# Optimization experiments

Measured on AMD Instinct MI355X. Metric: run time of the kernel, lower is better.

The kernel has to match this reference:

```python
import jax, jax.numpy as jnp
import numpy as np

FACTOR = 5  # sampling factor c

def setup_inputs() -> dict:
    key = jax.random.key(0)
    k1, k2, k3, k4 = jax.random.split(key, 4)
    B, H, L, D = 4, 8, 2048, 64
    u = min(max(1, FACTOR * int(np.ceil(np.log(L)))), L)  # sample_k = 40
    return {
        "queries": jax.random.normal(k1, (B, H, L, D), jnp.float32),
        "keys": jax.random.normal(k2, (B, H, L, D), jnp.float32),
        "values": jax.random.normal(k3, (B, H, L, D), jnp.float32),
        "index_sample": jax.random.randint(k4, (L, u), 0, L, jnp.int32),
    }

def reference(queries, keys, values, index_sample):
    B, H, L_Q, D = queries.shape
    L_K = keys.shape[2]
    scale = 1.0 / np.sqrt(D)
    U_part = min(max(1, FACTOR * int(np.ceil(np.log(L_K)))), L_Q)  # n_top queries

    # --- _prob_QK: sampled scores + sparsity measure ---
    # K_sample[b,h,q,s,:] = keys[b,h,index_sample[q,s],:]  -> (B,H,L_Q,u,D)
    K_sample = keys[:, :, index_sample, :]
    QK_sample = jnp.einsum('bhqd,bhqsd->bhqs', queries, K_sample)  # (B,H,L_Q,u)
    M = QK_sample.max(-1) - QK_sample.sum(-1) / L_K                # (B,H,L_Q)
    _, index = jax.lax.top_k(M, U_part)                            # (B,H,U)

    # --- initial context: mean of V for non-selected queries ---
    context = jnp.broadcast_to(values.mean(-2, keepdims=True), (B, H, L_Q, D))

    # --- full attention for the top-U queries only ---
    Q_reduce = jnp.take_along_axis(queries, index[..., None], axis=2)   # (B,H,U,D)
    scores = jnp.einsum('bhud,bhkd->bhuk', Q_reduce, keys) * scale      # (B,H,U,L_K)
    attn = jax.nn.softmax(scores, axis=-1)
    out = jnp.einsum('bhuk,bhkd->bhud', attn, values)                   # (B,H,U,D)

    # --- scatter selected outputs back into the mean context ---
    bi = jnp.arange(B)[:, None, None]
    hi = jnp.arange(H)[None, :, None]
    context = context.at[bi, hi, index].set(out)
    return context
```

## Files before the change

### kernel.cpp

```cpp
#include <hip/hip_runtime.h>
#include <math.h>

#define Bq 4
#define Hh 8
#define Lh 2048
#define Dh 64
#define BH (Bq*Hh)

__global__ __launch_bounds__(256) void kA_M(const float* __restrict__ Q,
                                            const float* __restrict__ K,
                                            const int* __restrict__ idxs,
                                            float* __restrict__ M, int u) {
    int bi = blockIdx.x;
    int xcd = bi & 7, slot = bi >> 3;
    int bh  = xcd * 4 + (slot >> 5);
    int qt  = slot & 31;
    int tid = threadIdx.x;
    int wave = tid >> 6, lane = tid & 63;
    int g = lane >> 2, c = lane & 3;
    int q = qt * 64 + wave * 16 + g;
    long gq = (long)bh * Lh + q;

    const float* qrow = Q + gq * Dh;
    float4 qf[4];
#pragma unroll
    for (int jj = 0; jj < 4; ++jj)
        qf[jj] = *(const float4*)(qrow + jj * 16 + c * 4);

    const float* kbase = K + (long)bh * Lh * Dh;
    const int* irow = idxs + q * u;
    float mx = -INFINITY, sm = 0.f;
    int s = 0;
    for (; s + 4 <= u; s += 4) {
        int4 ki = *(const int4*)(irow + s);
        const float* kp0 = kbase + (long)ki.x * Dh + c * 4;
        const float* kp1 = kbase + (long)ki.y * Dh + c * 4;
        const float* kp2 = kbase + (long)ki.z * Dh + c * 4;
        const float* kp3 = kbase + (long)ki.w * Dh + c * 4;
        float4 kf[4][4];
#pragma unroll
        for (int jj = 0; jj < 4; ++jj) {
            kf[0][jj] = *(const float4*)(kp0 + jj * 16);
            kf[1][jj] = *(const float4*)(kp1 + jj * 16);
            kf[2][jj] = *(const float4*)(kp2 + jj * 16);
            kf[3][jj] = *(const float4*)(kp3 + jj * 16);
        }
        float a[4];
#pragma unroll
        for (int r = 0; r < 4; ++r) {
            float ac = 0.f;
#pragma unroll
            for (int jj = 0; jj < 4; ++jj)
                ac += qf[jj].x*kf[r][jj].x + qf[jj].y*kf[r][jj].y
                    + qf[jj].z*kf[r][jj].z + qf[jj].w*kf[r][jj].w;
            a[r] = ac;
        }
#pragma unroll
        for (int r = 0; r < 4; ++r) {
            a[r] += __shfl_xor(a[r], 1);
            a[r] += __shfl_xor(a[r], 2);
            mx = fmaxf(mx, a[r]); sm += a[r];
        }
    }
    for (; s < u; ++s) {
        int ki = irow[s];
        const float* krow = kbase + (long)ki * Dh + c * 4;
        float acc = 0.f;
#pragma unroll
        for (int jj = 0; jj < 4; ++jj) {
            float4 kf = *(const float4*)(krow + jj * 16);
            acc += qf[jj].x*kf.x + qf[jj].y*kf.y + qf[jj].z*kf.z + qf[jj].w*kf.w;
        }
        acc += __shfl_xor(acc, 1);
        acc += __shfl_xor(acc, 2);
        mx = fmaxf(mx, acc); sm += acc;
    }
    if (c == 0) M[gq] = mx - sm * (1.0f / (float)Lh);
}

__global__ __launch_bounds__(256) void kB_topk(const float* __restrict__ M,
                                               int* __restrict__ topk, int U) {
    int bh = blockIdx.x, tid = threadIdx.x;
    const float* m = M + (long)bh * Lh;
    unsigned key[8];
#pragma unroll
    for (int j = 0; j < 8; ++j) {
        unsigned ub = __float_as_uint(m[tid + 256 * j]);
        key[j] = ub ^ ((ub >> 31) ? 0xFFFFFFFFu : 0x80000000u);
    }
    __shared__ unsigned hist[256];
    __shared__ unsigned prefix_s;
    __shared__ int need_s;
    if (tid == 0) { prefix_s = 0u; need_s = U; }

    for (int level = 3; level >= 0; --level) {
        int shift = level * 8;
        hist[tid] = 0u;
        __syncthreads();
        unsigned prefix = prefix_s;
        int need = need_s;
        unsigned pmask = (level == 3) ? 0u : (0xFFFFFFFFu << (shift + 8));
#pragma unroll
        for (int j = 0; j < 8; ++j)
            if ((key[j] & pmask) == prefix)
                atomicAdd(&hist[(key[j] >> shift) & 0xFF], 1u);
        __syncthreads();
        if (tid < 64) {
            int lane = tid;
            unsigned h0 = hist[lane*4+0], h1 = hist[lane*4+1],
                     h2 = hist[lane*4+2], h3 = hist[lane*4+3];
            unsigned lt = h0 + h1 + h2 + h3;
            unsigned ssum = lt;
#pragma unroll
            for (int off = 1; off < 64; off <<= 1) {
                unsigned t = __shfl_down(ssum, off);
                if (lane + off < 64) ssum += t;
            }
            unsigned sx  = ssum - lt;
            unsigned suf3 = sx  + h3;
            unsigned suf2 = suf3 + h2;
            unsigned suf1 = suf2 + h1;
            unsigned suf0 = suf1 + h0;
            int localb = -1; unsigned nxt = 0u;
            if      ((int)suf3 >= need) { localb = lane*4+3; nxt = sx;   }
            else if ((int)suf2 >= need) { localb = lane*4+2; nxt = suf3; }
            else if ((int)suf1 >= need) { localb = lane*4+1; nxt = suf2; }
            else if ((int)suf0 >= need) { localb = lane*4+0; nxt = suf1; }
            unsigned long long ball = __ballot(localb >= 0);
            int hilane = 63 - __clzll(ball);
            if (lane == hilane) {
                prefix_s = prefix | ((unsigned)localb << shift);
                need_s = need - (int)nxt;
            }
        }
        __syncthreads();
    }
    unsigned T = prefix_s;
    int r = need_s;
    __shared__ int cgt, ceq;
    if (tid == 0) { cgt = 0; ceq = 0; }
    __syncthreads();
    int* out = topk + bh * U;
#pragma unroll
    for (int j = 0; j < 8; ++j) {
        if (key[j] > T) { int p = atomicAdd(&cgt, 1); out[p] = tid + 256 * j; }
        else if (key[j] == T) { int e = atomicAdd(&ceq, 1); if (e < r) out[U - r + e] = tid + 256 * j; }
    }
}

__global__ __launch_bounds__(256) void kC_vpart(const float* __restrict__ V,
                                                float* __restrict__ vpart) {
    int bi = blockIdx.x;
    int xcd = bi & 7, slot = bi >> 3;
    int bh = xcd * 4 + (slot >> 3);
    int chunk = slot & 7;
    int tid = threadIdx.x;
    int d = tid & 63, r0 = tid >> 6;
    const float* vb = V + ((long)bh * Lh + chunk * 256) * Dh;
    float s = 0.f;
    for (int i = 0; i < 64; ++i) s += vb[(r0 + 4 * i) * Dh + d];
    __shared__ float part[4][64];
    part[r0][d] = s;
    __syncthreads();
    if (tid < 64) {
        float t = part[0][tid] + part[1][tid] + part[2][tid] + part[3][tid];
        vpart[(bh * 8 + chunk) * 64 + tid] = t;
    }
}

__global__ __launch_bounds__(256) void kE_fill(const float* __restrict__ vpart,
                                               float* __restrict__ ctx) {
    int tid = threadIdx.x;
    long base = (long)blockIdx.x * 1024;
    int bh = (int)(base >> 17);
    __shared__ float vm[64];
    if (tid < 64) {
        float s = 0.f;
#pragma unroll
        for (int c2 = 0; c2 < 8; ++c2) s += vpart[(bh * 8 + c2) * 64 + tid];
        vm[tid] = s * (1.0f / (float)Lh);
    }
    __syncthreads();
    float4 val = *(const float4*)(vm + ((tid * 4) & 63));
    *(float4*)(ctx + base + tid * 4) = val;
}

#define TK 64
__global__ __launch_bounds__(256) void kD_part(const float* __restrict__ Q,
                                               const float* __restrict__ K,
                                               const float* __restrict__ V,
                                               const int* __restrict__ topk,
                                               float* __restrict__ pm,
                                               float* __restrict__ pl,
                                               float* __restrict__ pacc,
                                               int U, int nch) {
    int bi = blockIdx.x;
    int xcd = bi & 7, slot = bi >> 3;
    int per = nch * 8;
    int bh = xcd * 4 + slot / per;
    int rest = slot % per;
    int uc = rest >> 3, kc = rest & 7;

    int tid = threadIdx.x;
    int wv = tid >> 6, lane = tid & 63;

    __shared__ float Qs[8 * 64];
    __shared__ float Ks[TK * 68];
    __shared__ float Ps[8 * 68];
    __shared__ float alph[8], mst[8], lst[8];
    __shared__ int   qidxs[8];
    float* accbuf = Ks;

    if (tid < 8) {
        int gu = uc * 8 + tid;
        qidxs[tid] = (gu < U) ? topk[bh * U + gu] : 0;
    }
    __syncthreads();
#pragma unroll
    for (int step = 0; step < 2; ++step) {
        int uu = step * 4 + wv;
        int row = qidxs[uu];
        Qs[uu * 64 + lane] = Q[((long)bh * Lh + row) * Dh + lane] * 0.125f;
    }

    int kq = lane, ug = wv;
    float mrun0 = -INFINITY, mrun1 = -INFINITY;
    float lrun0 = 0.f, lrun1 = 0.f;
    float accv[8] = {0.f,0.f,0.f,0.f,0.f,0.f,0.f,0.f};

    const long kvbase = (long)bh * Lh * Dh;
    const float4* Kg4 = (const float4*)(K + kvbase);
    const float*  Vg  = V + kvbase;
    int kbase0 = kc * 256;

    for (int t = 0; t < 4; ++t) {
        int t0 = kbase0 + t * TK;
        int f40 = t0 * (Dh / 4);
#pragma unroll
        for (int j = 0; j < 4; ++j) {
            int i = tid + 256 * j;
            float4 kv = Kg4[f40 + i];
            int row = i >> 4, col = i & 15;
            *(float4*)(&Ks[row * 68 + col * 4]) = kv;
        }
        __syncthreads();

        float s0 = 0.f, s1 = 0.f;
#pragma unroll
        for (int j16 = 0; j16 < 16; ++j16) {
            float4 kf = *(const float4*)(&Ks[kq * 68 + j16 * 4]);
            float4 qa = *(const float4*)(&Qs[(2 * ug + 0) * 64 + j16 * 4]);
            float4 qb = *(const float4*)(&Qs[(2 * ug + 1) * 64 + j16 * 4]);
            s0 += kf.x * qa.x + kf.y * qa.y + kf.z * qa.z + kf.w * qa.w;
            s1 += kf.x * qb.x + kf.y * qb.y + kf.z * qb.z + kf.w * qb.w;
        }
        float m0 = s0, m1 = s1;
#pragma unroll
        for (int off = 1; off < 64; off <<= 1) {
            m0 = fmaxf(m0, __shfl_xor(m0, off));
            m1 = fmaxf(m1, __shfl_xor(m1, off));
        }
        float mn0 = fmaxf(mrun0, m0), mn1 = fmaxf(mrun1, m1);
        float a0 = __expf(mrun0 - mn0), a1 = __expf(mrun1 - mn1);
        float p0 = __expf(s0 - mn0),  p1 = __expf(s1 - mn1);
        float ls0 = p0, ls1 = p1;
#pragma unroll
        for (int off = 1; off < 64; off <<= 1) {
            ls0 += __shfl_xor(ls0, off);
            ls1 += __shfl_xor(ls1, off);
        }
        lrun0 = a0 * lrun0 + ls0;  lrun1 = a1 * lrun1 + ls1;
        mrun0 = mn0;               mrun1 = mn1;
        Ps[(2 * ug + 0) * 68 + kq] = p0;
        Ps[(2 * ug + 1) * 68 + kq] = p1;
        if (lane == 0) { alph[2 * ug] = a0; alph[2 * ug + 1] = a1; }
        __syncthreads();

        float vk[16];
        int vrow0 = t0 + wv * 16;
#pragma unroll
        for (int k = 0; k < 16; ++k)
            vk[k] = Vg[(long)(vrow0 + k) * Dh + lane];
#pragma unroll
        for (int u2 = 0; u2 < 8; ++u2) {
            const float* pb = &Ps[u2 * 68 + wv * 16];
            float4 pA = *(const float4*)(pb + 0);
            float4 pB = *(const float4*)(pb + 4);
            float4 pC = *(const float4*)(pb + 8);
            float4 pD = *(const float4*)(pb + 12);
            float av = alph[u2];
            float ac = accv[u2] * av;
            ac += pA.x*vk[0]  + pA.y*vk[1]  + pA.z*vk[2]  + pA.w*vk[3];
            ac += pB.x*vk[4]  + pB.y*vk[5]  + pB.z*vk[6]  + pB.w*vk[7];
            ac += pC.x*vk[8]  + pC.y*vk[9]  + pC.z*vk[10] + pC.w*vk[11];
            ac += pD.x*vk[12] + pD.y*vk[13] + pD.z*vk[14] + pD.w*vk[15];
            accv[u2] = ac;
        }
    }

    if (lane == 0) {
        mst[2 * ug] = mrun0;     lst[2 * ug] = lrun0;
        mst[2 * ug + 1] = mrun1; lst[2 * ug + 1] = lrun1;
    }
#pragma unroll
    for (int u2 = 0; u2 < 8; ++u2)
        accbuf[wv * 512 + u2 * 64 + lane] = accv[u2];
    __syncthreads();

    int pbase = (bh * nch + uc) * 8;
    {
        int d = tid & 63, ua = tid >> 6;
#pragma unroll
        for (int h = 0; h < 2; ++h) {
            int u2 = ua + 4 * h;
            float o = accbuf[0 * 512 + u2 * 64 + d] + accbuf[1 * 512 + u2 * 64 + d]
                    + accbuf[2 * 512 + u2 * 64 + d] + accbuf[3 * 512 + u2 * 64 + d];
            pacc[((long)(pbase + u2) * 8 + kc) * 64 + d] = o;
        }
    }
    if (tid < 8) {
        int qp = (pbase + tid) * 8 + kc;
        pm[qp] = mst[tid];
        pl[qp] = lst[tid];
    }
}

__global__ __launch_bounds__(256) void kF_comb(const float* __restrict__ pm,
                                               const float* __restrict__ pl,
                                               const float* __restrict__ pacc,
                                               const int* __restrict__ topk,
                                               float* __restrict__ ctx,
                                               int U, int nch) {
    int bi = blockIdx.x;
    int bh = bi / nch, uc = bi % nch;
    int tid = threadIdx.x;
    int u = tid >> 5, t = tid & 31;
    int gu = uc * 8 + u;
    if (gu >= U) return;
    int qbase = (bh * nch + uc) * 8 + u;
    float m[8], l[8];
#pragma unroll
    for (int kc = 0; kc < 8; ++kc) { m[kc] = pm[qbase * 8 + kc]; l[kc] = pl[qbase * 8 + kc]; }
    float gm = m[0];
#pragma unroll
    for (int kc = 1; kc < 8; ++kc) gm = fmaxf(gm, m[kc]);
    float w[8]; float gl = 0.f;
#pragma unroll
    for (int kc = 0; kc < 8; ++kc) { w[kc] = __expf(m[kc] - gm); gl += l[kc] * w[kc]; }
    float inv = 1.0f / gl;
    float o0 = 0.f, o1 = 0.f;
#pragma unroll
    for (int kc = 0; kc < 8; ++kc) {
        const float* a = pacc + ((long)qbase * 8 + kc) * 64;
        o0 += a[t] * w[kc];
        o1 += a[t + 32] * w[kc];
    }
    int row = topk[bh * U + gu];
    float* crow = ctx + ((long)bh * Lh + row) * Dh;
    crow[t]      = o0 * inv;
    crow[t + 32] = o1 * inv;
}

extern "C" void kernel_launch(void* const* d_in, const int* in_sizes, int n_in,
                              void* d_out, int out_size, void* d_ws, size_t ws_size,
                              hipStream_t stream) {
    const float* Q    = (const float*)d_in[0];
    const float* K    = (const float*)d_in[1];
    const float* V    = (const float*)d_in[2];
    const int*   idxs = (const int*)d_in[3];
    float* ctx = (float*)d_out;

    int u = in_sizes[3] / Lh;
    int U = u;
    int nch = (U + 7) / 8;

    float* wsf   = (float*)d_ws;
    float* M     = wsf;
    int*   topk  = (int*)(wsf + 65536);
    float* vpart = wsf + 65536 + 2048;
    float* pm    = wsf + 83968;
    float* pl    = pm + 32 * nch * 8 * 8;
    float* pacc  = pl + 32 * nch * 8 * 8;

    kA_M    <<<1024,           256, 0, stream>>>(Q, K, idxs, M, u);
    kC_vpart<<<256,            256, 0, stream>>>(V, vpart);
    kB_topk <<<BH,             256, 0, stream>>>(M, topk, U);
    kE_fill <<<4096,           256, 0, stream>>>(vpart, ctx);
    kD_part <<<BH * nch * 8,   256, 0, stream>>>(Q, K, V, topk, pm, pl, pacc, U, nch);
    kF_comb <<<BH * nch,       256, 0, stream>>>(pm, pl, pacc, topk, ctx, U, nch);
}
```

Baseline: 156.7 us.

## Merge independent kernels into combined launches and split sampled-score work across blocks

```diff
diff --git a/kernel.cpp b/kernel.cpp
--- a/kernel.cpp
+++ b/kernel.cpp
@@ -7,85 +7,130 @@
 #define Dh 64
 #define BH (Bq*Hh)
 
-__global__ __launch_bounds__(256) void kA_M(const float* __restrict__ Q,
-                                            const float* __restrict__ K,
-                                            const int* __restrict__ idxs,
-                                            float* __restrict__ M, int u) {
+__global__ __launch_bounds__(256) void kAC(const float* __restrict__ Q,
+                                           const float* __restrict__ K,
+                                           const float* __restrict__ V,
+                                           const int* __restrict__ idxs,
+                                           float2* __restrict__ M2,
+                                           float* __restrict__ vpart, int u) {
     int bi = blockIdx.x;
-    int xcd = bi & 7, slot = bi >> 3;
-    int bh  = xcd * 4 + (slot >> 5);
-    int qt  = slot & 31;
     int tid = threadIdx.x;
-    int wave = tid >> 6, lane = tid & 63;
-    int g = lane >> 2, c = lane & 3;
-    int q = qt * 64 + wave * 16 + g;
-    long gq = (long)bh * Lh + q;
-
-    const float* qrow = Q + gq * Dh;
-    float4 qf[4];
-#pragma unroll
-    for (int jj = 0; jj < 4; ++jj)
-        qf[jj] = *(const float4*)(qrow + jj * 16 + c * 4);
-
-    const float* kbase = K + (long)bh * Lh * Dh;
-    const int* irow = idxs + q * u;
-    float mx = -INFINITY, sm = 0.f;
-    int s = 0;
-    for (; s + 4 <= u; s += 4) {
-        int4 ki = *(const int4*)(irow + s);
-        const float* kp0 = kbase + (long)ki.x * Dh + c * 4;
-        const float* kp1 = kbase + (long)ki.y * Dh + c * 4;
-        const float* kp2 = kbase + (long)ki.z * Dh + c * 4;
-        const float* kp3 = kbase + (long)ki.w * Dh + c * 4;
-        float4 kf[4][4];
-#pragma unroll
-        for (int jj = 0; jj < 4; ++jj) {
-            kf[0][jj] = *(const float4*)(kp0 + jj * 16);
-            kf[1][jj] = *(const float4*)(kp1 + jj * 16);
-            kf[2][jj] = *(const float4*)(kp2 + jj * 16);
-            kf[3][jj] = *(const float4*)(kp3 + jj * 16);
-        }
-        float a[4];
-#pragma unroll
-        for (int r = 0; r < 4; ++r) {
-            float ac = 0.f;
-#pragma unroll
-            for (int jj = 0; jj < 4; ++jj)
-                ac += qf[jj].x*kf[r][jj].x + qf[jj].y*kf[r][jj].y
-                    + qf[jj].z*kf[r][jj].z + qf[jj].w*kf[r][jj].w;
-            a[r] = ac;
-        }
-#pragma unroll
-        for (int r = 0; r < 4; ++r) {
-            a[r] += __shfl_xor(a[r], 1);
-            a[r] += __shfl_xor(a[r], 2);
-            mx = fmaxf(mx, a[r]); sm += a[r];
-        }
-    }
-    for (; s < u; ++s) {
-        int ki = irow[s];
-        const float* krow = kbase + (long)ki * Dh + c * 4;
-        float acc = 0.f;
-#pragma unroll
-        for (int jj = 0; jj < 4; ++jj) {
-            float4 kf = *(const float4*)(krow + jj * 16);
-            acc += qf[jj].x*kf.x + qf[jj].y*kf.y + qf[jj].z*kf.z + qf[jj].w*kf.w;
-        }
-        acc += __shfl_xor(acc, 1);
-        acc += __shfl_xor(acc, 2);
-        mx = fmaxf(mx, acc); sm += acc;
-    }
-    if (c == 0) M[gq] = mx - sm * (1.0f / (float)Lh);
-}
-
-__global__ __launch_bounds__(256) void kB_topk(const float* __restrict__ M,
-                                               int* __restrict__ topk, int U) {
-    int bh = blockIdx.x, tid = threadIdx.x;
-    const float* m = M + (long)bh * Lh;
+    if (bi < 2048) {
+        int xcd = bi & 7, slot = bi >> 3;
+        int bh  = xcd * 4 + (slot >> 6);
+        int qt  = (slot >> 1) & 31;
+        int half = slot & 1;
+        int wave = tid >> 6, lane = tid & 63;
+        int g = lane >> 2, c = lane & 3;
+        int q = qt * 64 + wave * 16 + g;
+        long gq = (long)bh * Lh + q;
+
+        const float* qrow = Q + gq * Dh;
+        float4 qf[4];
+#pragma unroll
+        for (int jj = 0; jj < 4; ++jj)
+            qf[jj] = *(const float4*)(qrow + jj * 16 + c * 4);
+
+        int cnt1 = u >> 1;
+        int c0 = (half == 0) ? (u - cnt1) : cnt1;
+        const int* irow = idxs + (long)q * u + (half ? (u - cnt1) : 0);
+        const float* kbase = K + (long)bh * Lh * Dh;
+
+        float mx = -INFINITY, sm = 0.f;
+        int s = 0;
+        for (; s + 4 <= c0; s += 4) {
+            int i0 = irow[s], i1 = irow[s+1], i2 = irow[s+2], i3 = irow[s+3];
+            const float* kp0 = kbase + (long)i0 * Dh + c * 4;
+            const float* kp1 = kbase + (long)i1 * Dh + c * 4;
+            const float* kp2 = kbase + (long)i2 * Dh + c * 4;
+            const float* kp3 = kbase + (long)i3 * Dh + c * 4;
+            float4 kf[4][4];
+#pragma unroll
+            for (int jj = 0; jj < 4; ++jj) {
+                kf[0][jj] = *(const float4*)(kp0 + jj * 16);
+                kf[1][jj] = *(const float4*)(kp1 + jj * 16);
+                kf[2][jj] = *(const float4*)(kp2 + jj * 16);
+                kf[3][jj] = *(const float4*)(kp3 + jj * 16);
+            }
+            float a[4];
+#pragma unroll
+            for (int r = 0; r < 4; ++r) {
+                float ac = 0.f;
+#pragma unroll
+                for (int jj = 0; jj < 4; ++jj)
+                    ac += qf[jj].x*kf[r][jj].x + qf[jj].y*kf[r][jj].y
+                        + qf[jj].z*kf[r][jj].z + qf[jj].w*kf[r][jj].w;
+                a[r] = ac;
+            }
+#pragma unroll
+            for (int r = 0; r < 4; ++r) {
+                a[r] += __shfl_xor(a[r], 1);
+                a[r] += __shfl_xor(a[r], 2);
+                mx = fmaxf(mx, a[r]); sm += a[r];
+            }
+        }
+        for (; s < c0; ++s) {
+            int ki = irow[s];
+            const float* krow = kbase + (long)ki * Dh + c * 4;
+            float acc = 0.f;
+#pragma unroll
+            for (int jj = 0; jj < 4; ++jj) {
+                float4 kf = *(const float4*)(krow + jj * 16);
+                acc += qf[jj].x*kf.x + qf[jj].y*kf.y + qf[jj].z*kf.z + qf[jj].w*kf.w;
+            }
+            acc += __shfl_xor(acc, 1);
+            acc += __shfl_xor(acc, 2);
+            mx = fmaxf(mx, acc); sm += acc;
+        }
+        if (c == 0) M2[gq * 2 + half] = make_float2(mx, sm);
+    } else {
+        int b2 = bi - 2048;
+        int xcd = b2 & 7, slot = b2 >> 3;
+        int bh = xcd * 4 + (slot >> 3);
+        int chunk = slot & 7;
+        int d = tid & 63, r0 = tid >> 6;
+        const float* vb = V + ((long)bh * Lh + chunk * 256) * Dh;
+        float s = 0.f;
+        for (int i = 0; i < 64; ++i) s += vb[(r0 + 4 * i) * Dh + d];
+        __shared__ float part[4][64];
+        part[r0][d] = s;
+        __syncthreads();
+        if (tid < 64) {
+            float t = part[0][tid] + part[1][tid] + part[2][tid] + part[3][tid];
+            vpart[(bh * 8 + chunk) * 64 + tid] = t;
+        }
+    }
+}
+
+__global__ __launch_bounds__(256) void kBE(const float2* __restrict__ M2,
+                                           const float* __restrict__ vpart,
+                                           int* __restrict__ topk,
+                                           float* __restrict__ ctx, int U) {
+    int bi = blockIdx.x;
+    int tid = threadIdx.x;
+    if (bi < 4096) {
+        long base = (long)bi * 1024;
+        int bh = (int)(base >> 17);
+        __shared__ float vm[64];
+        if (tid < 64) {
+            float s = 0.f;
+#pragma unroll
+            for (int c2 = 0; c2 < 8; ++c2) s += vpart[(bh * 8 + c2) * 64 + tid];
+            vm[tid] = s * (1.0f / (float)Lh);
+        }
+        __syncthreads();
+        float4 val = *(const float4*)(vm + ((tid * 4) & 63));
+        *(float4*)(ctx + base + tid * 4) = val;
+        return;
+    }
+    int bh = bi - 4096;
     unsigned key[8];
 #pragma unroll
     for (int j = 0; j < 8; ++j) {
-        unsigned ub = __float_as_uint(m[tid + 256 * j]);
+        long q = (long)bh * Lh + tid + 256 * j;
+        float4 mm = *(const float4*)(&M2[q * 2]);
+        float Mv = fmaxf(mm.x, mm.z) - (mm.y + mm.w) * (1.0f / (float)Lh);
+        unsigned ub = __float_as_uint(Mv);
         key[j] = ub ^ ((ub >> 31) ? 0xFFFFFFFFu : 0x80000000u);
     }
     __shared__ unsigned hist[256];
@@ -148,43 +193,6 @@
     }
 }
 
-__global__ __launch_bounds__(256) void kC_vpart(const float* __restrict__ V,
-                                                float* __restrict__ vpart) {
-    int bi = blockIdx.x;
-    int xcd = bi & 7, slot = bi >> 3;
-    int bh = xcd * 4 + (slot >> 3);
-    int chunk = slot & 7;
-    int tid = threadIdx.x;
-    int d = tid & 63, r0 = tid >> 6;
-    const float* vb = V + ((long)bh * Lh + chunk * 256) * Dh;
-    float s = 0.f;
-    for (int i = 0; i < 64; ++i) s += vb[(r0 + 4 * i) * Dh + d];
-    __shared__ float part[4][64];
-    part[r0][d] = s;
-    __syncthreads();
-    if (tid < 64) {
-        float t = part[0][tid] + part[1][tid] + part[2][tid] + part[3][tid];
-        vpart[(bh * 8 + chunk) * 64 + tid] = t;
-    }
-}
-
-__global__ __launch_bounds__(256) void kE_fill(const float* __restrict__ vpart,
-                                               float* __restrict__ ctx) {
-    int tid = threadIdx.x;
-    long base = (long)blockIdx.x * 1024;
-    int bh = (int)(base >> 17);
-    __shared__ float vm[64];
-    if (tid < 64) {
-        float s = 0.f;
-#pragma unroll
-        for (int c2 = 0; c2 < 8; ++c2) s += vpart[(bh * 8 + c2) * 64 + tid];
-        vm[tid] = s * (1.0f / (float)Lh);
-    }
-    __syncthreads();
-    float4 val = *(const float4*)(vm + ((tid * 4) & 63));
-    *(float4*)(ctx + base + tid * 4) = val;
-}
-
 #define TK 64
 __global__ __launch_bounds__(256) void kD_part(const float* __restrict__ Q,
                                                const float* __restrict__ K,
@@ -205,11 +213,11 @@
     int wv = tid >> 6, lane = tid & 63;
 
     __shared__ float Qs[8 * 64];
-    __shared__ float Ks[TK * 68];
-    __shared__ float Ps[8 * 68];
-    __shared__ float alph[8], mst[8], lst[8];
+    __shared__ float Ps[2][8 * 68];
+    __shared__ float alph[2][8];
+    __shared__ float mst[8], lst[8];
     __shared__ int   qidxs[8];
-    float* accbuf = Ks;
+    __shared__ float accbuf[4 * 512];
 
     if (tid < 8) {
         int gu = uc * 8 + tid;
@@ -222,6 +230,7 @@
         int row = qidxs[uu];
         Qs[uu * 64 + lane] = Q[((long)bh * Lh + row) * Dh + lane] * 0.125f;
     }
+    __syncthreads();
 
     int kq = lane, ug = wv;
     float mrun0 = -INFINITY, mrun1 = -INFINITY;
@@ -229,26 +238,18 @@
     float accv[8] = {0.f,0.f,0.f,0.f,0.f,0.f,0.f,0.f};
 
     const long kvbase = (long)bh * Lh * Dh;
-    const float4* Kg4 = (const float4*)(K + kvbase);
-    const float*  Vg  = V + kvbase;
+    const float* Kg = K + kvbase;
+    const float* Vg = V + kvbase;
     int kbase0 = kc * 256;
 
     for (int t = 0; t < 4; ++t) {
         int t0 = kbase0 + t * TK;
-        int f40 = t0 * (Dh / 4);
-#pragma unroll
-        for (int j = 0; j < 4; ++j) {
-            int i = tid + 256 * j;
-            float4 kv = Kg4[f40 + i];
-            int row = i >> 4, col = i & 15;
-            *(float4*)(&Ks[row * 68 + col * 4]) = kv;
-        }
-        __syncthreads();
-
+        int pp = t & 1;
+        const float4* kr = (const float4*)(Kg + (long)(t0 + kq) * Dh);
         float s0 = 0.f, s1 = 0.f;
 #pragma unroll
         for (int j16 = 0; j16 < 16; ++j16) {
-            float4 kf = *(const float4*)(&Ks[kq * 68 + j16 * 4]);
+            float4 kf = kr[j16];
             float4 qa = *(const float4*)(&Qs[(2 * ug + 0) * 64 + j16 * 4]);
             float4 qb = *(const float4*)(&Qs[(2 * ug + 1) * 64 + j16 * 4]);
             s0 += kf.x * qa.x + kf.y * qa.y + kf.z * qa.z + kf.w * qa.w;
@@ -271,9 +272,9 @@
         }
         lrun0 = a0 * lrun0 + ls0;  lrun1 = a1 * lrun1 + ls1;
         mrun0 = mn0;               mrun1 = mn1;
-        Ps[(2 * ug + 0) * 68 + kq] = p0;
-        Ps[(2 * ug + 1) * 68 + kq] = p1;
-        if (lane == 0) { alph[2 * ug] = a0; alph[2 * ug + 1] = a1; }
+        Ps[pp][(2 * ug + 0) * 68 + kq] = p0;
+        Ps[pp][(2 * ug + 1) * 68 + kq] = p1;
+        if (lane == 0) { alph[pp][2 * ug] = a0; alph[pp][2 * ug + 1] = a1; }
         __syncthreads();
 
         float vk[16];
@@ -283,12 +284,12 @@
             vk[k] = Vg[(long)(vrow0 + k) * Dh + lane];
 #pragma unroll
         for (int u2 = 0; u2 < 8; ++u2) {
-            const float* pb = &Ps[u2 * 68 + wv * 16];
+            const float* pb = &Ps[pp][u2 * 68 + wv * 16];
             float4 pA = *(const float4*)(pb + 0);
             float4 pB = *(const float4*)(pb + 4);
             float4 pC = *(const float4*)(pb + 8);
             float4 pD = *(const float4*)(pb + 12);
-            float av = alph[u2];
+            float av = alph[pp][u2];
             float ac = accv[u2] * av;
             ac += pA.x*vk[0]  + pA.y*vk[1]  + pA.z*vk[2]  + pA.w*vk[3];
             ac += pB.x*vk[4]  + pB.y*vk[5]  + pB.z*vk[6]  + pB.w*vk[7];
@@ -374,18 +375,16 @@
     int U = u;
     int nch = (U + 7) / 8;
 
-    float* wsf   = (float*)d_ws;
-    float* M     = wsf;
-    int*   topk  = (int*)(wsf + 65536);
-    float* vpart = wsf + 65536 + 2048;
-    float* pm    = wsf + 83968;
-    float* pl    = pm + 32 * nch * 8 * 8;
-    float* pacc  = pl + 32 * nch * 8 * 8;
-
-    kA_M    <<<1024,           256, 0, stream>>>(Q, K, idxs, M, u);
-    kC_vpart<<<256,            256, 0, stream>>>(V, vpart);
-    kB_topk <<<BH,             256, 0, stream>>>(M, topk, U);
-    kE_fill <<<4096,           256, 0, stream>>>(vpart, ctx);
-    kD_part <<<BH * nch * 8,   256, 0, stream>>>(Q, K, V, topk, pm, pl, pacc, U, nch);
-    kF_comb <<<BH * nch,       256, 0, stream>>>(pm, pl, pacc, topk, ctx, U, nch);
-}
+    float*  wsf   = (float*)d_ws;
+    float2* M2    = (float2*)wsf;
+    int*    topk  = (int*)(wsf + 262144);
+    float*  vpart = wsf + 262144 + 2048;
+    float*  pm    = wsf + 280576;
+    float*  pl    = pm + 32 * nch * 8 * 8;
+    float*  pacc  = pl + 32 * nch * 8 * 8;
+
+    kAC    <<<2304,         256, 0, stream>>>(Q, K, V, idxs, M2, vpart, u);
+    kBE    <<<4128,         256, 0, stream>>>(M2, vpart, topk, ctx, U);
+    kD_part<<<BH * nch * 8, 256, 0, stream>>>(Q, K, V, topk, pm, pl, pacc, U, nch);
+    kF_comb<<<BH * nch,     256, 0, stream>>>(pm, pl, pacc, topk, ctx, U, nch);
+}
```

New measurement: 177.5 us. 1.13x slower.
